# Optimization experiments

Measured on AMD Instinct MI355X. Metric: run time of the kernel, lower is better.

## Reference

```python
import jax, jax.numpy as jnp
import numpy as np

B, C, H, W = 16, 256, 64, 64   # img feature map -> S = H*W = 4096 query tokens
L, TXT = 256, 256              # text tokens / text_dim
NH, HD = 4, 64                 # fusion_num_heads, fusion_head_dim -> embed_dim 256
E = NH * HD


def layernorm(x, w, b, eps=1e-5):
    mu = x.mean(-1, keepdims=True)
    var = ((x - mu) ** 2).mean(-1, keepdims=True)
    return (x - mu) * jax.lax.rsqrt(var + eps) * w + b


def setup_inputs() -> dict:
    key = jax.random.key(0)
    ks = jax.random.split(key, 10)
    s = 0.02  # xavier-ish init scale
    return {
        "img_x": jax.random.normal(ks[0], (B, C, H, W), jnp.float32),
        "refs": jax.random.normal(ks[1], (B, L, TXT), jnp.float32),
        "masks": jax.random.bernoulli(ks[2], 0.2, (B, L)),  # True = padded token
        "ref_embeds": jax.random.normal(ks[3], (B, C), jnp.float32),
        "ln_img_w": jnp.ones((C,), jnp.float32),
        "ln_img_b": jnp.zeros((C,), jnp.float32),
        "ln_txt_w": jnp.ones((TXT,), jnp.float32),
        "ln_txt_b": jnp.zeros((TXT,), jnp.float32),
        "Wq": jax.random.normal(ks[4], (C, E), jnp.float32) * s,
        "bq": jnp.zeros((E,), jnp.float32),
        "Wk": jax.random.normal(ks[5], (TXT, E), jnp.float32) * s,
        "bk": jnp.zeros((E,), jnp.float32),
        "Wv": jax.random.normal(ks[6], (TXT, E), jnp.float32) * s,
        "bv": jnp.zeros((E,), jnp.float32),
        "Wo": jax.random.normal(ks[7], (E, C), jnp.float32) * s,
        "bo": jnp.zeros((C,), jnp.float32),
        "W_ada": jax.random.normal(ks[8], (C, 3 * C), jnp.float32) * s,
        "b_ada": jnp.zeros((3 * C,), jnp.float32),
    }


def reference(img_x, refs, masks, ref_embeds,
              ln_img_w, ln_img_b, ln_txt_w, ln_txt_b,
              Wq, bq, Wk, bk, Wv, bv, Wo, bo, W_ada, b_ada):
    B_, C_, H_, W_ = img_x.shape
    x = img_x.reshape(B_, C_, H_ * W_).transpose(0, 2, 1)  # [B, S, C]

    qn = layernorm(x, ln_img_w, ln_img_b)
    kn = layernorm(refs, ln_txt_w, ln_txt_b)

    q = (qn @ Wq + bq).reshape(B_, -1, NH, HD).astype(jnp.bfloat16)
    k = (kn @ Wk + bk).reshape(B_, -1, NH, HD).astype(jnp.bfloat16)
    v = (kn @ Wv + bv).reshape(B_, -1, NH, HD).astype(jnp.bfloat16)

    scale = 1.0 / np.sqrt(HD).astype(np.float32)
    scores = jnp.einsum('bqhd,bkhd->bhqk', q, k).astype(jnp.float32) * scale
    valid = ~masks  # unpad_input keeps keys where (~masks)==1
    scores = jnp.where(valid[:, None, None, :], scores, -jnp.inf)
    p = jax.nn.softmax(scores, axis=-1).astype(jnp.bfloat16)
    o = jnp.einsum('bhqk,bkhd->bqhd', p, v).reshape(B_, -1, E).astype(jnp.float32)
    attn = o @ Wo + bo  # [B, S, C]

    # AdaLN shift/scale/gate modulation from ref_embeds
    mod = jax.nn.silu(ref_embeds) @ W_ada + b_ada  # [B, 3C]
    shift, sc, gate = jnp.split(mod, 3, axis=1)
    attn = gate[:, None, :] * (attn * (1.0 + sc[:, None, :]) + shift[:, None, :])

    out = (attn + x).transpose(0, 2, 1).reshape(B_, C_, H_, W_)
    return out
```

## Files before the change

kernel.cpp:

```cpp
#include <hip/hip_runtime.h>
#include <hip/hip_bf16.h>

#define NB 16
#define NC 256
#define NS 4096
#define NL 256
#define NE 256
#define NHH 4
#define HDD 64

using bf16 = __hip_bfloat16;
typedef short bf16x8 __attribute__((ext_vector_type(8)));
typedef float f32x4 __attribute__((ext_vector_type(4)));

__device__ __forceinline__ float bf16r(float x) {
    return __bfloat162float(__float2bfloat16(x));
}
__device__ __forceinline__ float rsqrt_nr(float x) {
    float r = rsqrtf(x);
    r = r * (1.5f - 0.5f * x * r * r);
    return r;
}
__device__ __forceinline__ ushort us(float x) {
    bf16 h = __float2bfloat16(x);
    return *(ushort*)&h;
}

__global__ void __launch_bounds__(256) wt_kernel(const float* __restrict__ Wq,
                                                 const float* __restrict__ Wk,
                                                 const float* __restrict__ Wv,
                                                 const float* __restrict__ Wo,
                                                 ushort* __restrict__ wqt,
                                                 ushort* __restrict__ wkt,
                                                 ushort* __restrict__ wvt,
                                                 ushort* __restrict__ wot) {
    int m = blockIdx.x >> 3, strip = blockIdx.x & 7;
    const float* W = (m == 0) ? Wq : (m == 1) ? Wk : (m == 2) ? Wv : Wo;
    ushort* Wt = (m == 0) ? wqt : (m == 1) ? wkt : (m == 2) ? wvt : wot;
    int t = threadIdx.x;
    __shared__ float tile[32 * 257];
    int in0 = strip * 32;
    for (int i = 0; i < 32; i++) tile[i * 257 + t] = W[(size_t)(in0 + i) * 256 + t];
    __syncthreads();
    ushort vals[32];
#pragma unroll
    for (int i = 0; i < 32; i++) vals[i] = us(tile[i * 257 + t]);
#pragma unroll
    for (int i = 0; i < 32; i += 8)
        *(uint4*)(Wt + (size_t)t * 256 + in0 + i) = *(const uint4*)(vals + i);
}

__global__ void __launch_bounds__(256) mod_kernel(const float* __restrict__ ref_embeds,
                                                  const float* __restrict__ W_ada,
                                                  const float* __restrict__ b_ada,
                                                  float* __restrict__ mod) {
    int b = blockIdx.x / 12, jc = blockIdx.x % 12;
    int t = threadIdx.x;
    __shared__ float silu[NC];
    __shared__ float part[256];
    float x = ref_embeds[b * NC + t];
    silu[t] = x / (1.f + expf(-x));
    __syncthreads();
    int j = jc * 64 + (t & 63);
    int cq = t >> 6;
    float acc = 0.f;
#pragma unroll 8
    for (int c = cq * 64; c < cq * 64 + 64; c++) acc += silu[c] * W_ada[c * 3 * NC + j];
    part[t] = acc;
    __syncthreads();
    if (t < 64) {
        mod[b * 3 * NC + j] = part[t] + part[t + 64] + part[t + 128] + part[t + 192] + b_ada[j];
    }
}

__global__ void __launch_bounds__(256) kv_kernel(const float* __restrict__ refs,
                                                 const float* __restrict__ lw,
                                                 const float* __restrict__ lb,
                                                 const ushort* __restrict__ Wkt,
                                                 const float* __restrict__ bk,
                                                 const ushort* __restrict__ Wvt,
                                                 const float* __restrict__ bv,
                                                 bf16* __restrict__ kbuf,
                                                 bf16* __restrict__ vbuf) {
    int blk = blockIdx.x;
    int b = blk >> 2;
    int l0 = (blk & 3) << 6;
    int t = threadIdx.x;
    __shared__ ushort At[64 * 264];
    __shared__ float lws[NC], lbs[NC];
    lws[t] = lw[t];
    lbs[t] = lb[t];
    int r = t >> 2, j = t & 3;
    const float* rp = refs + ((size_t)(b * NL + l0 + r)) * NC + j * 64;
    float v[64];
#pragma unroll
    for (int i = 0; i < 16; i++) {
        float4 f = *(const float4*)(rp + i * 4);
        v[i * 4 + 0] = f.x; v[i * 4 + 1] = f.y; v[i * 4 + 2] = f.z; v[i * 4 + 3] = f.w;
    }
    float s = 0;
#pragma unroll
    for (int i = 0; i < 64; i++) s += v[i];
    s += __shfl_xor(s, 1, 64);
    s += __shfl_xor(s, 2, 64);
    float mu = s * (1.f / NC);
    float vr = 0;
#pragma unroll
    for (int i = 0; i < 64; i++) {
        float d = v[i] - mu;
        vr += d * d;
    }
    vr += __shfl_xor(vr, 1, 64);
    vr += __shfl_xor(vr, 2, 64);
    float rs = rsqrt_nr(vr * (1.f / NC) + 1e-5f);
    __syncthreads();
    ushort nv[64];
#pragma unroll
    for (int i = 0; i < 64; i++) {
        int c = j * 64 + i;
        nv[i] = us((v[i] - mu) * rs * lws[c] + lbs[c]);
    }
#pragma unroll
    for (int i = 0; i < 64; i += 4)
        *(uint2*)(At + r * 264 + j * 64 + i) = *(const uint2*)(nv + i);
    __syncthreads();

    int w = t >> 6, lane = t & 63, l16 = lane & 15, quad = lane >> 4;
    int r0 = w * 16;
    f32x4 zero = {0.f, 0.f, 0.f, 0.f};
    f32x4 ak[16], av[16];
#pragma unroll
    for (int et = 0; et < 16; et++) { ak[et] = zero; av[et] = zero; }
    const ushort* ap = At + (r0 + l16) * 264 + quad * 8;
    const ushort* kp = Wkt + (size_t)l16 * NC + quad * 8;
    const ushort* vp = Wvt + (size_t)l16 * NC + quad * 8;
#pragma unroll
    for (int kc = 0; kc < 8; kc++) {
        bf16x8 a = *(const bf16x8*)(ap + kc * 32);
#pragma unroll
        for (int et = 0; et < 16; et++) {
            bf16x8 bbk = *(const bf16x8*)(kp + (size_t)et * 16 * NC + kc * 32);
            ak[et] = __builtin_amdgcn_mfma_f32_16x16x32_bf16(a, bbk, ak[et], 0, 0, 0);
        }
#pragma unroll
        for (int et = 0; et < 16; et++) {
            bf16x8 bbv = *(const bf16x8*)(vp + (size_t)et * 16 * NC + kc * 32);
            av[et] = __builtin_amdgcn_mfma_f32_16x16x32_bf16(a, bbv, av[et], 0, 0, 0);
        }
    }
#pragma unroll
    for (int et = 0; et < 16; et++) {
        int e = et * 16 + l16;
        float bkv = bk[e], bvv = bv[e];
#pragma unroll
        for (int rr = 0; rr < 4; rr++) {
            size_t row = (size_t)(b * NL + l0 + r0 + quad * 4 + rr);
            kbuf[row * NE + e] = __float2bfloat16(ak[et][rr] + bkv);
            vbuf[row * NE + e] = __float2bfloat16(av[et][rr] + bvv);
        }
    }
}

__global__ void __launch_bounds__(256) vt_kernel(const bf16* __restrict__ vbuf,
                                                 ushort* __restrict__ vtbuf) {
    int bh = blockIdx.x;
    int b = bh >> 2, h = bh & 3;
    int t = threadIdx.x;
    __shared__ ushort tile[64 * 264];
    const ushort* vp = (const ushort*)vbuf + ((size_t)b * NL) * NE + h * HDD;
#pragma unroll
    for (int i = 0; i < 8; i++) {
        int l = i * 32 + (t >> 3);
        uint4 v = *(const uint4*)(vp + (size_t)l * NE + (t & 7) * 8);
        const ushort* v8 = (const ushort*)&v;
#pragma unroll
        for (int j = 0; j < 8; j++) tile[((t & 7) * 8 + j) * 264 + l] = v8[j];
    }
    __syncthreads();
    ushort* op = vtbuf + (size_t)bh * HDD * NL;
#pragma unroll
    for (int i = 0; i < 8; i++) {
        int d = i * 8 + (t >> 5);
        int l = (t & 31) * 8;
        *(uint4*)(op + (size_t)d * NL + l) = *(const uint4*)(tile + d * 264 + l);
    }
}

__global__ void __launch_bounds__(256, 2) q_kernel(const float* __restrict__ img_x,
                                                   const float* __restrict__ lw,
                                                   const float* __restrict__ lb,
                                                   const ushort* __restrict__ Wqt,
                                                   const float* __restrict__ bq,
                                                   bf16* __restrict__ qbuf) {
    int blk = blockIdx.x;
    int b = blk >> 7;
    int s0 = (blk & 127) << 5;
    int t = threadIdx.x;
    int sl = t & 31, ch = t >> 5;
    __shared__ __attribute__((aligned(16))) char At[32 * 512];
    __shared__ float part_s[256], part_q[256];
    __shared__ float mu_s[32], rs_s[32];

    const float* xp = img_x + ((size_t)b * NC) * NS + s0 + sl;
    float v[32];
#pragma unroll
    for (int i = 0; i < 32; i++) v[i] = xp[(size_t)(ch * 32 + i) * NS];
    float sacc = 0.f, qacc = 0.f;
#pragma unroll
    for (int i = 0; i < 32; i++) {
        sacc += v[i];
        qacc += v[i] * v[i];
    }
    part_s[t] = sacc;
    part_q[t] = qacc;
    __syncthreads();
    if (t < 32) {
        float sm = 0.f, sq = 0.f;
#pragma unroll
        for (int jj = 0; jj < 8; jj++) {
            sm += part_s[jj * 32 + t];
            sq += part_q[jj * 32 + t];
        }
        float mu = sm * (1.f / NC);
        mu_s[t] = mu;
        rs_s[t] = rsqrt_nr(sq * (1.f / NC) - mu * mu + 1e-5f);
    }
    __syncthreads();
    float mu = mu_s[sl], rs = rs_s[sl];
    int swz = (sl & 7) << 4;
#pragma unroll
    for (int i = 0; i < 4; i++) {
        int cb = ch * 32 + i * 8;
        float4 lwa = *(const float4*)(lw + cb);
        float4 lwb = *(const float4*)(lw + cb + 4);
        float4 lba = *(const float4*)(lb + cb);
        float4 lbb = *(const float4*)(lb + cb + 4);
        float wv[8] = {lwa.x, lwa.y, lwa.z, lwa.w, lwb.x, lwb.y, lwb.z, lwb.w};
        float bv_[8] = {lba.x, lba.y, lba.z, lba.w, lbb.x, lbb.y, lbb.z, lbb.w};
        uint u[4];
#pragma unroll
        for (int jj = 0; jj < 4; jj++) {
            float x0 = (v[i * 8 + jj * 2] - mu) * rs * wv[jj * 2] + bv_[jj * 2];
            float x1 = (v[i * 8 + jj * 2 + 1] - mu) * rs * wv[jj * 2 + 1] + bv_[jj * 2 + 1];
            u[jj] = (uint)us(x0) | ((uint)us(x1) << 16);
        }
        *(uint4*)(At + ((sl * 512 + ch * 64 + i * 16) ^ swz)) = *(const uint4*)u;
    }
    __syncthreads();

    int w = t >> 6, lane = t & 63, l16 = lane & 15, quad = lane >> 4;
    int r0 = (w & 1) * 16, e0 = (w >> 1) * 128;
    int arow = r0 + l16;
    int aswz = (arow & 7) << 4;
    f32x4 zero = {0.f, 0.f, 0.f, 0.f};
    f32x4 acc[8];
#pragma unroll
    for (int dt = 0; dt < 8; dt++) acc[dt] = zero;
    const ushort* bp = Wqt + (size_t)(e0 + l16) * NC + quad * 8;
#pragma unroll
    for (int kc = 0; kc < 8; kc++) {
        bf16x8 a = *(const bf16x8*)(At + ((arow * 512 + kc * 64 + quad * 16) ^ aswz));
        bf16x8 bb[8];
#pragma unroll
        for (int dt = 0; dt < 8; dt++)
            bb[dt] = *(const bf16x8*)(bp + (size_t)dt * 16 * NC + kc * 32);
#pragma unroll
        for (int dt = 0; dt < 8; dt++)
            acc[dt] = __builtin_amdgcn_mfma_f32_16x16x32_bf16(a, bb[dt], acc[dt], 0, 0, 0);
    }
#pragma unroll
    for (int dt = 0; dt < 8; dt++) {
        int e = e0 + dt * 16 + l16;
        float bqv = bq[e];
#pragma unroll
        for (int r = 0; r < 4; r++) {
            int s = s0 + r0 + quad * 4 + r;
            qbuf[((size_t)b * NS + s) * NE + e] = __float2bfloat16(acc[dt][r] + bqv);
        }
    }
}

__global__ void __launch_bounds__(256) attn_kernel(const bf16* __restrict__ qbuf,
                                                   const bf16* __restrict__ kbuf,
                                                   const ushort* __restrict__ vtbuf,
                                                   const int* __restrict__ masks,
                                                   bf16* __restrict__ obuf) {
    int blk = blockIdx.x;
    int chunk = blk & 7;
    int bh = blk >> 3;
    int h = bh & 3;
    int b = bh >> 2;
    int t = threadIdx.x;
    int w = t >> 6, lane = t & 63;
    int l16 = lane & 15, quad = lane >> 4;

    __shared__ __attribute__((aligned(16))) char sK[32768];
    __shared__ __attribute__((aligned(16))) char sV[32768];

    const char* kgb = (const char*)kbuf + ((size_t)(b * NL) * NE + h * HDD) * 2;
    const char* vgb = (const char*)vtbuf + (size_t)bh * HDD * NL * 2;
#pragma unroll
    for (int i = 0; i < 8; i++) {
        int g = t * 16 + i * 4096;
        uint4 kv = *(const uint4*)(kgb + (size_t)(g >> 7) * 512 + (g & 127));
        *(uint4*)(sK + (g ^ (((g >> 7) & 7) << 4))) = kv;
        uint4 vv = *(const uint4*)(vgb + g);
        *(uint4*)(sV + (g ^ (((g >> 9) & 7) << 4))) = vv;
    }

    const int* mp = masks + b * NL;
    unsigned long long bal0 = __ballot(mp[lane] != 0);
    unsigned long long bal1 = __ballot(mp[64 + lane] != 0);
    unsigned long long bal2 = __ballot(mp[128 + lane] != 0);
    unsigned long long bal3 = __ballot(mp[192 + lane] != 0);
    uint mw0 = 0, mw1 = 0;
#pragma unroll
    for (int kk = 0; kk < 4; kk++) {
        mw0 |= (uint)((bal0 >> (16 * kk + 4 * quad)) & 15ULL) << (4 * kk);
        mw0 |= (uint)((bal1 >> (16 * kk + 4 * quad)) & 15ULL) << (4 * kk + 16);
        mw1 |= (uint)((bal2 >> (16 * kk + 4 * quad)) & 15ULL) << (4 * kk);
        mw1 |= (uint)((bal3 >> (16 * kk + 4 * quad)) & 15ULL) << (4 * kk + 16);
    }

    int sbase = chunk * 512;
    const ushort* qp0 = (const ushort*)qbuf +
                        ((size_t)(b * NS + sbase + w * 16 + l16)) * NE + h * HDD + quad * 8;
    bf16x8 af0 = *(const bf16x8*)qp0;
    bf16x8 af1 = *(const bf16x8*)(qp0 + 32);

    __syncthreads();

    int kswz = (l16 & 7) << 4;
    int src0 = l16 + 32 * (quad & 1);
    int src1 = src0 + 16;
    bool ahi = quad >= 2;

    for (int it = 0; it < 8; it++) {
        int s0 = sbase + it * 64;
        bf16x8 nf0, nf1;
        if (it < 7) {
            const ushort* qn = qp0 + (size_t)(it + 1) * 64 * NE;
            nf0 = *(const bf16x8*)qn;
            nf1 = *(const bf16x8*)(qn + 32);
        }

        f32x4 acc[16];
#pragma unroll
        for (int kt = 0; kt < 16; kt++) {
            int row = kt * 16 + l16;
            bf16x8 kf0 = *(const bf16x8*)(sK + ((row * 128 + quad * 16) ^ kswz));
            bf16x8 kf1 = *(const bf16x8*)(sK + ((row * 128 + quad * 16 + 64) ^ kswz));
            f32x4 z = {0.f, 0.f, 0.f, 0.f};
            z = __builtin_amdgcn_mfma_f32_16x16x32_bf16(kf0, af0, z, 0, 0, 0);
            acc[kt] = __builtin_amdgcn_mfma_f32_16x16x32_bf16(kf1, af1, z, 0, 0, 0);
        }

        float srow = 0.f;
#pragma unroll
        for (int kt = 0; kt < 16; kt++) {
            uint nib = ((kt < 8) ? mw0 : mw1) >> (4 * (kt & 7));
#pragma unroll
            for (int r = 0; r < 4; r++) {
                float p = exp2f(bf16r(acc[kt][r]) * 0.18033688f);
                p = ((nib >> r) & 1) ? 0.f : p;
                acc[kt][r] = p;
                srow += p;
            }
        }
        srow += __shfl_xor(srow, 16, 64);
        srow += __shfl_xor(srow, 32, 64);
        float inv = 1.f / srow;

        uint Wloc[32];
#pragma unroll
        for (int kt = 0; kt < 16; kt++) {
            Wloc[2 * kt] = (uint)us(acc[kt][0] * inv) | ((uint)us(acc[kt][1] * inv) << 16);
            Wloc[2 * kt + 1] = (uint)us(acc[kt][2] * inv) | ((uint)us(acc[kt][3] * inv) << 16);
        }

        f32x4 oacc[4];
#pragma unroll
        for (int dt = 0; dt < 4; dt++) oacc[dt] = f32x4{0.f, 0.f, 0.f, 0.f};
#pragma unroll
        for (int kc = 0; kc < 8; kc++) {
            uint a0 = (uint)__shfl((int)Wloc[4 * kc + 0], src0, 64);
            uint b0 = (uint)__shfl((int)Wloc[4 * kc + 2], src0, 64);
            uint a1 = (uint)__shfl((int)Wloc[4 * kc + 1], src0, 64);
            uint b1 = (uint)__shfl((int)Wloc[4 * kc + 3], src0, 64);
            uint a2 = (uint)__shfl((int)Wloc[4 * kc + 0], src1, 64);
            uint b2 = (uint)__shfl((int)Wloc[4 * kc + 2], src1, 64);
            uint a3 = (uint)__shfl((int)Wloc[4 * kc + 1], src1, 64);
            uint b3 = (uint)__shfl((int)Wloc[4 * kc + 3], src1, 64);
            union { uint u[4]; bf16x8 v; } pu;
            pu.u[0] = ahi ? b0 : a0;
            pu.u[1] = ahi ? b1 : a1;
            pu.u[2] = ahi ? b2 : a2;
            pu.u[3] = ahi ? b3 : a3;
#pragma unroll
            for (int dt = 0; dt < 4; dt++) {
                int row = dt * 16 + l16;
                bf16x8 vb = *(const bf16x8*)(sV + ((row * 512 + kc * 64 + quad * 16) ^ kswz));
                oacc[dt] = __builtin_amdgcn_mfma_f32_16x16x32_bf16(pu.v, vb, oacc[dt], 0, 0, 0);
            }
        }

        bf16* op = obuf + ((size_t)(b * NS + s0 + w * 16 + quad * 4)) * NE + h * HDD + l16;
#pragma unroll
        for (int dt = 0; dt < 4; dt++) {
#pragma unroll
            for (int r = 0; r < 4; r++)
                op[(size_t)r * NE + dt * 16] = __float2bfloat16(oacc[dt][r]);
        }
        if (it < 7) { af0 = nf0; af1 = nf1; }
    }
}

__global__ void __launch_bounds__(256) out_kernel(const bf16* __restrict__ obuf,
                                                  const ushort* __restrict__ Wot,
                                                  const float* __restrict__ bo,
                                                  const float* __restrict__ mod,
                                                  const float* __restrict__ img_x,
                                                  float* __restrict__ out) {
    int blk = blockIdx.x;
    int b = blk >> 6;
    int s0 = (blk & 63) << 6;
    int t = threadIdx.x;
    int w = t >> 6, lane = t & 63, l16 = lane & 15, quad = lane >> 4;
    int c0 = w * 64;

    f32x4 zero = {0.f, 0.f, 0.f, 0.f};
    f32x4 acc[4][4];
#pragma unroll
    for (int ct = 0; ct < 4; ct++)
#pragma unroll
        for (int st = 0; st < 4; st++) acc[ct][st] = zero;

    const ushort* ap0 = Wot + (size_t)(c0 + l16) * NE + quad * 8;
    const ushort* bp0 = (const ushort*)obuf + ((size_t)(b * NS + s0 + l16)) * NE + quad * 8;
#pragma unroll
    for (int kc = 0; kc < 8; kc++) {
        bf16x8 a[4], bb[4];
#pragma unroll
        for (int ct = 0; ct < 4; ct++)
            a[ct] = *(const bf16x8*)(ap0 + (size_t)ct * 16 * NE + kc * 32);
#pragma unroll
        for (int st = 0; st < 4; st++)
            bb[st] = *(const bf16x8*)(bp0 + (size_t)st * 16 * NE + kc * 32);
#pragma unroll
        for (int ct = 0; ct < 4; ct++)
#pragma unroll
            for (int st = 0; st < 4; st++)
                acc[ct][st] = __builtin_amdgcn_mfma_f32_16x16x32_bf16(a[ct], bb[st], acc[ct][st], 0, 0, 0);
    }

#pragma unroll
    for (int ct = 0; ct < 4; ct++) {
#pragma unroll
        for (int r = 0; r < 4; r++) {
            int c = c0 + ct * 16 + quad * 4 + r;
            float sh = mod[b * 768 + c];
            float scv = mod[b * 768 + 256 + c];
            float ga = mod[b * 768 + 512 + c];
            float bov = bo[c];
            const float* xr = img_x + ((size_t)(b * NC + c)) * NS + s0;
            float* orow = out + ((size_t)(b * NC + c)) * NS + s0;
#pragma unroll
            for (int st = 0; st < 4; st++) {
                float y = ga * ((acc[ct][st][r] + bov) * (1.f + scv) + sh) + xr[st * 16 + l16];
                orow[st * 16 + l16] = y;
            }
        }
    }
}

extern "C" void kernel_launch(void* const* d_in, const int* in_sizes, int n_in,
                              void* d_out, int out_size, void* d_ws, size_t ws_size,
                              hipStream_t stream) {
    const float* img_x = (const float*)d_in[0];
    const float* refs = (const float*)d_in[1];
    const int* masks = (const int*)d_in[2];
    const float* ref_embeds = (const float*)d_in[3];
    const float* ln_img_w = (const float*)d_in[4];
    const float* ln_img_b = (const float*)d_in[5];
    const float* ln_txt_w = (const float*)d_in[6];
    const float* ln_txt_b = (const float*)d_in[7];
    const float* Wq = (const float*)d_in[8];
    const float* bq = (const float*)d_in[9];
    const float* Wk = (const float*)d_in[10];
    const float* bk = (const float*)d_in[11];
    const float* Wv = (const float*)d_in[12];
    const float* bv = (const float*)d_in[13];
    const float* Wo = (const float*)d_in[14];
    const float* bo = (const float*)d_in[15];
    const float* W_ada = (const float*)d_in[16];
    const float* b_ada = (const float*)d_in[17];
    float* out = (float*)d_out;

    char* ws = (char*)d_ws;
    float* mod = (float*)ws;
    ushort* wqt = (ushort*)(ws + 49152);
    ushort* wkt = (ushort*)(ws + 180224);
    ushort* wvt = (ushort*)(ws + 311296);
    ushort* wot = (ushort*)(ws + 442368);
    bf16* kbuf = (bf16*)(ws + 573440);
    ushort* vtbuf = (ushort*)(ws + 2670592);
    bf16* qbuf = (bf16*)(ws + 4767744);
    bf16* obuf = (bf16*)(ws + 38322176);
    bf16* vbuf = obuf;

    hipLaunchKernelGGL(wt_kernel, dim3(32), dim3(256), 0, stream,
                       Wq, Wk, Wv, Wo, wqt, wkt, wvt, wot);
    hipLaunchKernelGGL(mod_kernel, dim3(NB * 12), dim3(256), 0, stream,
                       ref_embeds, W_ada, b_ada, mod);
    hipLaunchKernelGGL(kv_kernel, dim3(NB * 4), dim3(256), 0, stream,
                       refs, ln_txt_w, ln_txt_b, wkt, bk, wvt, bv, kbuf, vbuf);
    hipLaunchKernelGGL(vt_kernel, dim3(NB * NHH), dim3(256), 0, stream,
                       vbuf, vtbuf);
    hipLaunchKernelGGL(q_kernel, dim3(NB * (NS / 32)), dim3(256), 0, stream,
                       img_x, ln_img_w, ln_img_b, wqt, bq, qbuf);
    hipLaunchKernelGGL(attn_kernel, dim3(NB * NHH * 8), dim3(256), 0, stream,
                       qbuf, kbuf, vtbuf, masks, obuf);
    hipLaunchKernelGGL(out_kernel, dim3(NB * (NS / 64)), dim3(256), 0, stream,
                       obuf, wot, bo, mod, img_x, out);
}
```

Before: 395.1 us.

## Retile q_kernel to 64 tokens per block with vectorized float4 image loads

```diff
diff --git a/kernel.cpp b/kernel.cpp
--- a/kernel.cpp
+++ b/kernel.cpp
@@ -193,89 +193,96 @@
                                                    const float* __restrict__ bq,
                                                    bf16* __restrict__ qbuf) {
     int blk = blockIdx.x;
-    int b = blk >> 7;
-    int s0 = (blk & 127) << 5;
-    int t = threadIdx.x;
-    int sl = t & 31, ch = t >> 5;
-    __shared__ __attribute__((aligned(16))) char At[32 * 512];
-    __shared__ float part_s[256], part_q[256];
-    __shared__ float mu_s[32], rs_s[32];
-
-    const float* xp = img_x + ((size_t)b * NC) * NS + s0 + sl;
-    float v[32];
-#pragma unroll
-    for (int i = 0; i < 32; i++) v[i] = xp[(size_t)(ch * 32 + i) * NS];
-    float sacc = 0.f, qacc = 0.f;
-#pragma unroll
-    for (int i = 0; i < 32; i++) {
-        sacc += v[i];
-        qacc += v[i] * v[i];
-    }
-    part_s[t] = sacc;
-    part_q[t] = qacc;
-    __syncthreads();
-    if (t < 32) {
+    int b = blk >> 6;
+    int s0 = (blk & 63) << 6;
+    int t = threadIdx.x;
+    int cg = t >> 4, s4 = t & 15;
+
+    __shared__ __attribute__((aligned(16))) char At[64 * 512];
+    __shared__ float part_s[16 * 64], part_q[16 * 64];
+    __shared__ float mu_s[64], rs_s[64];
+    __shared__ float lws[NC], lbs[NC];
+    lws[t] = lw[t];
+    lbs[t] = lb[t];
+
+    const float* xp = img_x + ((size_t)b * NC) * NS + s0 + s4 * 4;
+    float4 v4[16];
+#pragma unroll
+    for (int i = 0; i < 16; i++) v4[i] = *(const float4*)(xp + (size_t)(i * 16 + cg) * NS);
+    float ss0 = 0.f, ss1 = 0.f, ss2 = 0.f, ss3 = 0.f;
+    float qq0 = 0.f, qq1 = 0.f, qq2 = 0.f, qq3 = 0.f;
+#pragma unroll
+    for (int i = 0; i < 16; i++) {
+        ss0 += v4[i].x; qq0 += v4[i].x * v4[i].x;
+        ss1 += v4[i].y; qq1 += v4[i].y * v4[i].y;
+        ss2 += v4[i].z; qq2 += v4[i].z * v4[i].z;
+        ss3 += v4[i].w; qq3 += v4[i].w * v4[i].w;
+    }
+    float4 ssv = {ss0, ss1, ss2, ss3};
+    float4 qqv = {qq0, qq1, qq2, qq3};
+    *(float4*)&part_s[cg * 64 + s4 * 4] = ssv;
+    *(float4*)&part_q[cg * 64 + s4 * 4] = qqv;
+    __syncthreads();
+
+    if (t < 64) {
         float sm = 0.f, sq = 0.f;
 #pragma unroll
-        for (int jj = 0; jj < 8; jj++) {
-            sm += part_s[jj * 32 + t];
-            sq += part_q[jj * 32 + t];
+        for (int g = 0; g < 16; g++) {
+            sm += part_s[g * 64 + t];
+            sq += part_q[g * 64 + t];
         }
         float mu = sm * (1.f / NC);
         mu_s[t] = mu;
         rs_s[t] = rsqrt_nr(sq * (1.f / NC) - mu * mu + 1e-5f);
     }
     __syncthreads();
-    float mu = mu_s[sl], rs = rs_s[sl];
-    int swz = (sl & 7) << 4;
-#pragma unroll
-    for (int i = 0; i < 4; i++) {
-        int cb = ch * 32 + i * 8;
-        float4 lwa = *(const float4*)(lw + cb);
-        float4 lwb = *(const float4*)(lw + cb + 4);
-        float4 lba = *(const float4*)(lb + cb);
-        float4 lbb = *(const float4*)(lb + cb + 4);
-        float wv[8] = {lwa.x, lwa.y, lwa.z, lwa.w, lwb.x, lwb.y, lwb.z, lwb.w};
-        float bv_[8] = {lba.x, lba.y, lba.z, lba.w, lbb.x, lbb.y, lbb.z, lbb.w};
-        uint u[4];
-#pragma unroll
-        for (int jj = 0; jj < 4; jj++) {
-            float x0 = (v[i * 8 + jj * 2] - mu) * rs * wv[jj * 2] + bv_[jj * 2];
-            float x1 = (v[i * 8 + jj * 2 + 1] - mu) * rs * wv[jj * 2 + 1] + bv_[jj * 2 + 1];
-            u[jj] = (uint)us(x0) | ((uint)us(x1) << 16);
-        }
-        *(uint4*)(At + ((sl * 512 + ch * 64 + i * 16) ^ swz)) = *(const uint4*)u;
+
+    float mus[4], rss[4];
+#pragma unroll
+    for (int r = 0; r < 4; r++) {
+        mus[r] = mu_s[s4 * 4 + r];
+        rss[r] = rs_s[s4 * 4 + r];
+    }
+#pragma unroll
+    for (int i = 0; i < 16; i++) {
+        int c = i * 16 + cg;
+        float wv = lws[c], bv_ = lbs[c];
+        float xs[4] = {v4[i].x, v4[i].y, v4[i].z, v4[i].w};
+#pragma unroll
+        for (int r = 0; r < 4; r++) {
+            int s = s4 * 4 + r;
+            int sw = (((s ^ (s >> 3)) & 7) << 4);
+            *(ushort*)(At + ((s * 512 + c * 2) ^ sw)) = us((xs[r] - mus[r]) * rss[r] * wv + bv_);
+        }
     }
     __syncthreads();
 
     int w = t >> 6, lane = t & 63, l16 = lane & 15, quad = lane >> 4;
-    int r0 = (w & 1) * 16, e0 = (w >> 1) * 128;
+    int r0 = w * 16;
     int arow = r0 + l16;
-    int aswz = (arow & 7) << 4;
+    int asw = (((arow ^ (arow >> 3)) & 7) << 4);
     f32x4 zero = {0.f, 0.f, 0.f, 0.f};
-    f32x4 acc[8];
-#pragma unroll
-    for (int dt = 0; dt < 8; dt++) acc[dt] = zero;
-    const ushort* bp = Wqt + (size_t)(e0 + l16) * NC + quad * 8;
+    f32x4 acc[16];
+#pragma unroll
+    for (int et = 0; et < 16; et++) acc[et] = zero;
+    const ushort* bp = Wqt + (size_t)l16 * NC + quad * 8;
 #pragma unroll
     for (int kc = 0; kc < 8; kc++) {
-        bf16x8 a = *(const bf16x8*)(At + ((arow * 512 + kc * 64 + quad * 16) ^ aswz));
-        bf16x8 bb[8];
-#pragma unroll
-        for (int dt = 0; dt < 8; dt++)
-            bb[dt] = *(const bf16x8*)(bp + (size_t)dt * 16 * NC + kc * 32);
-#pragma unroll
-        for (int dt = 0; dt < 8; dt++)
-            acc[dt] = __builtin_amdgcn_mfma_f32_16x16x32_bf16(a, bb[dt], acc[dt], 0, 0, 0);
-    }
-#pragma unroll
-    for (int dt = 0; dt < 8; dt++) {
-        int e = e0 + dt * 16 + l16;
+        bf16x8 a = *(const bf16x8*)(At + ((arow * 512 + kc * 64 + quad * 16) ^ asw));
+#pragma unroll
+        for (int et = 0; et < 16; et++) {
+            bf16x8 bb = *(const bf16x8*)(bp + (size_t)et * 16 * NC + kc * 32);
+            acc[et] = __builtin_amdgcn_mfma_f32_16x16x32_bf16(a, bb, acc[et], 0, 0, 0);
+        }
+    }
+#pragma unroll
+    for (int et = 0; et < 16; et++) {
+        int e = et * 16 + l16;
         float bqv = bq[e];
 #pragma unroll
-        for (int r = 0; r < 4; r++) {
-            int s = s0 + r0 + quad * 4 + r;
-            qbuf[((size_t)b * NS + s) * NE + e] = __float2bfloat16(acc[dt][r] + bqv);
+        for (int rr = 0; rr < 4; rr++) {
+            int s = s0 + r0 + quad * 4 + rr;
+            qbuf[((size_t)b * NS + s) * NE + e] = __float2bfloat16(acc[et][rr] + bqv);
         }
     }
 }
@@ -516,7 +523,7 @@
                        refs, ln_txt_w, ln_txt_b, wkt, bk, wvt, bv, kbuf, vbuf);
     hipLaunchKernelGGL(vt_kernel, dim3(NB * NHH), dim3(256), 0, stream,
                        vbuf, vtbuf);
-    hipLaunchKernelGGL(q_kernel, dim3(NB * (NS / 32)), dim3(256), 0, stream,
+    hipLaunchKernelGGL(q_kernel, dim3(NB * 64), dim3(256), 0, stream,
                        img_x, ln_img_w, ln_img_b, wqt, bq, qbuf);
     hipLaunchKernelGGL(attn_kernel, dim3(NB * NHH * 8), dim3(256), 0, stream,
                        qbuf, kbuf, vtbuf, masks, obuf);
```

Measured after the change: 401.7 us. About the same (+1.7%).
